# Kernel tuning notes

Measured on AMD Instinct MI355X. Metric: run time of the kernel, lower is better.

Reference implementation:

```python
import jax, jax.numpy as jnp
import numpy as np

B, S, E, H, D, NE, R = 2, 2048, 2048, 16, 128, 8, 16
HALF = D // 2
THETA = 10000.0


def setup_inputs() -> dict:
    key = jax.random.key(0)
    ks = jax.random.split(key, 18)

    def w(k, shape, fan_in):
        return jax.random.normal(k, shape, jnp.float32) / np.float32(np.sqrt(fan_in))

    inp = {
        "x": jax.random.normal(ks[0], (B, S, E), jnp.float32),
        "expert_mask": jax.random.uniform(ks[1], (B, S, NE), dtype=jnp.float32),
    }
    for i, n in enumerate(("q", "k", "v")):
        inp["W" + n] = w(ks[2 + 3 * i], (H * D, E), E)
        inp["b" + n] = jnp.zeros((H * D,), jnp.float32)
        inp["A" + n] = w(ks[3 + 3 * i], (NE, R, E), E)
        inp["B" + n] = w(ks[4 + 3 * i], (H * D, NE, R), R)
    inp["Wo"] = w(ks[11], (E, H * D), H * D)
    inp["bo"] = jnp.zeros((E,), jnp.float32)
    inp["Ao"] = w(ks[12], (NE, R, H * D), H * D)
    inp["Bo"] = w(ks[13], (E, NE, R), R)
    return inp


def routed_linear(x, W, b, A, Bm, mask):
    """MaybeRoutedLinear: dense base + expert-routed low-rank path gated by mask [B,S,NE]."""
    y = jnp.einsum("bsi,oi->bso", x, W) + b
    h = jnp.einsum("bsi,eri->bser", x, A) * mask[..., None]  # [B,S,NE,R]
    return y + jnp.einsum("bser,oer->bso", h, Bm)


def apply_rope(t):
    """Llama-style rotary embedding. t: [B,S,H,D]."""
    inv_freq = 1.0 / (THETA ** (jnp.arange(0, D, 2, dtype=jnp.float32) / D))  # [D/2]
    freqs = jnp.arange(S, dtype=jnp.float32)[:, None] * inv_freq[None, :]  # [S,D/2]
    cos = jnp.concatenate([jnp.cos(freqs)] * 2, -1)[None, :, None, :]  # [1,S,1,D]
    sin = jnp.concatenate([jnp.sin(freqs)] * 2, -1)[None, :, None, :]
    rot = jnp.concatenate([-t[..., HALF:], t[..., :HALF]], -1)
    return t * cos + rot * sin


def reference(x, expert_mask, Wq, bq, Aq, Bq, Wk, bk, Ak, Bk, Wv, bv, Av, Bv, Wo, bo, Ao, Bo):
    q = routed_linear(x, Wq, bq, Aq, Bq, expert_mask).reshape(B, S, H, D)
    k = routed_linear(x, Wk, bk, Ak, Bk, expert_mask).reshape(B, S, H, D)
    v = routed_linear(x, Wv, bv, Av, Bv, expert_mask).reshape(B, S, H, D)
    q = apply_rope(q)
    k = apply_rope(k)
    scores = jnp.einsum("bqhd,bkhd->bhqk", q, k) / jnp.float32(np.sqrt(D))
    causal = jnp.tril(jnp.ones((S, S), dtype=bool))
    scores = jnp.where(causal[None, None], scores, jnp.finfo(scores.dtype).min)
    probs = jax.nn.softmax(scores, axis=-1)
    o = jnp.einsum("bhqk,bkhd->bqhd", probs, v).reshape(B, S, H * D)
    return routed_linear(o, Wo, bo, Ao, Bo, expert_mask)
```

## Files before the change

kernel.cpp:

```cpp
#include <hip/hip_runtime.h>


#define B_ 2
#define S_ 2048
#define E_ 2048
#define H_ 16
#define D_ 128
#define NE_ 8
#define R_ 16
#define HD_ 2048
#define M_ 4096
#define KL_ 128

typedef unsigned short u16;
typedef unsigned int u32;
typedef __attribute__((ext_vector_type(8))) short bf16x8;
typedef __attribute__((ext_vector_type(4))) float f32x4;

typedef const __attribute__((address_space(1))) void gvoid_t;
typedef __attribute__((address_space(3))) void svoid_t;

__device__ __forceinline__ float bf2f(u16 u) {
    union { u32 i; float f; } v; v.i = ((u32)u) << 16; return v.f;
}
__device__ __forceinline__ u16 f2bf(float f) {
    union { float f; u32 i; } v; v.f = f;
    u32 x = v.i;
    return (u16)((x + 0x7fffu + ((x >> 16) & 1u)) >> 16);
}
__device__ __forceinline__ float ldf(const void* p, size_t i, int f) {
    return f ? ((const float*)p)[i] : bf2f(((const u16*)p)[i]);
}
__device__ __forceinline__ float4 ld4(const void* p, size_t i, int f) {
    if (f) return *(const float4*)((const float*)p + i);
    ushort4 v = *(const ushort4*)((const u16*)p + i);
    return make_float4(bf2f(v.x), bf2f(v.y), bf2f(v.z), bf2f(v.w));
}

__global__ void k_detect(const void* __restrict__ x, int* __restrict__ flags) {
    __shared__ int votes[2];
    int tid = threadIdx.x;
    if (tid < 2) votes[tid] = 0;
    __syncthreads();
    const u32* p = (const u32*)x;
    int bad = 0, tot = 0;
    for (int i = tid; i < 4096; i += 64) {
        u32 lo = p[i] & 0xffffu;
        if (lo) {
            tot++;
            int e = (int)((lo >> 7) & 0xffu);
            if (e < 100 || e > 150) bad++;
        }
    }
    atomicAdd(&votes[0], bad);
    atomicAdd(&votes[1], tot);
    __syncthreads();
    if (tid == 0) flags[0] = (votes[1] > 0 && votes[0] * 10 > votes[1] * 3) ? 1 : 0;
}

__global__ void k_cvt(const void* __restrict__ src, u16* __restrict__ dst, int n,
                      const int* __restrict__ flags) {
    int fin = flags[0];
    int i = (blockIdx.x * 256 + threadIdx.x) * 4;
    if (i >= n) return;
    float4 v = ld4(src, i, fin);
    ushort4 o;
    o.x = f2bf(v.x); o.y = f2bf(v.y); o.z = f2bf(v.z); o.w = f2bf(v.w);
    *(ushort4*)(dst + i) = o;
}

__global__ void k_cvtf(const float* __restrict__ src, u16* __restrict__ dst, int n) {
    int i = (blockIdx.x * 256 + threadIdx.x) * 4;
    if (i >= n) return;
    float4 v = *(const float4*)(src + i);
    ushort4 o;
    o.x = f2bf(v.x); o.y = f2bf(v.y); o.z = f2bf(v.z); o.w = f2bf(v.w);
    *(ushort4*)(dst + i) = o;
}

__global__ void k_zero(float4* __restrict__ p, int n4) {
    int i = blockIdx.x * 256 + threadIdx.x;
    if (i < n4) p[i] = make_float4(0.f, 0.f, 0.f, 0.f);
}

#define NX_  8388608L
#define NA1_ 262144L
#define NW_  4194304L
__global__ void k_cvt_all(
    const void* __restrict__ x,
    const void* __restrict__ Aq, const void* __restrict__ Ak,
    const void* __restrict__ Av, const void* __restrict__ Ao,
    const void* __restrict__ Bq, const void* __restrict__ Bk,
    const void* __restrict__ Bv, const void* __restrict__ Bo,
    const void* __restrict__ Wq, const void* __restrict__ Wk,
    const void* __restrict__ Wv,
    u16* __restrict__ Xb, u16* __restrict__ Acat, u16* __restrict__ Bmcat,
    u16* __restrict__ Wcat,
    const int* __restrict__ flags) {
    int fin = flags[0];
    long i = (long)(blockIdx.x * 256 + threadIdx.x) * 4;
    const void* src; u16* dst; long off;
    if (i < NX_) { src = x; dst = Xb; off = i; }
    else if (i < NX_ + 4 * NA1_) {
        long j = i - NX_; int p = (int)(j >> 18); off = j & (NA1_ - 1);
        src = (p == 0) ? Aq : (p == 1) ? Ak : (p == 2) ? Av : Ao;
        dst = Acat + (long)p * NA1_;
    } else if (i < NX_ + 8 * NA1_) {
        long j = i - NX_ - 4 * NA1_; int p = (int)(j >> 18); off = j & (NA1_ - 1);
        src = (p == 0) ? Bq : (p == 1) ? Bk : (p == 2) ? Bv : Bo;
        dst = Bmcat + (long)p * NA1_;
    } else {
        long j = i - NX_ - 8 * NA1_; int p = (int)(j / NW_); off = j - (long)p * NW_;
        src = (p == 0) ? Wq : (p == 1) ? Wk : Wv;
        dst = Wcat + (long)p * NW_;
    }
    float4 v = ld4(src, off, fin);
    ushort4 o;
    o.x = f2bf(v.x); o.y = f2bf(v.y); o.z = f2bf(v.z); o.w = f2bf(v.w);
    *(ushort4*)(dst + off) = o;
}

#define BM_ 128
#define BN_ 128
#define BK_ 64

__global__ __launch_bounds__(256, 2) void k_gemm_sk(
    const u16* __restrict__ A, int lda,
    const u16* __restrict__ Bw, int ldb, int K,
    const void* __restrict__ mask,
    float* __restrict__ Cf, int ldc,
    const int* __restrict__ flags) {
    __shared__ __align__(16) u16 As[BM_ * BK_];
    __shared__ __align__(16) u16 Bs[BN_ * BK_];
    int fin = flags[0];
    int tid = threadIdx.x;
    int w = tid >> 6, lane = tid & 63;
    int l15 = lane & 15, quad = lane >> 4;
    int wm = w >> 1, wn = w & 1;
    int m0 = blockIdx.y * BM_, n0 = blockIdx.x * BN_;
    int lrow = lane >> 3;
    int lcol = (lane & 7) * 8;

    f32x4 acc[4][4];
#pragma unroll
    for (int mt = 0; mt < 4; mt++)
#pragma unroll
        for (int nt = 0; nt < 4; nt++)
#pragma unroll
            for (int r = 0; r < 4; r++) acc[mt][nt][r] = 0.f;

    int iters = (K / BK_) / gridDim.z;
    int it0 = blockIdx.z * iters;
    for (int it = it0; it < it0 + iters; it++) {
        int kb = it * BK_;
        __syncthreads();
#pragma unroll
        for (int i = 0; i < 4; i++) {
            int rowb = (w * 4 + i) * 8;
            int r = rowb + lrow;
            __builtin_amdgcn_global_load_lds(
                (gvoid_t*)(A + (size_t)(m0 + r) * lda + kb + lcol),
                (svoid_t*)(As + rowb * BK_), 16, 0, 0);
            __builtin_amdgcn_global_load_lds(
                (gvoid_t*)(Bw + (size_t)(n0 + r) * ldb + kb + lcol),
                (svoid_t*)(Bs + rowb * BK_), 16, 0, 0);
        }
        __syncthreads();
#pragma unroll
        for (int kk = 0; kk < 2; kk++) {
            int ko = kk * 32 + quad * 8;
            bf16x8 af[4], bf[4];
#pragma unroll
            for (int mt = 0; mt < 4; mt++)
                af[mt] = *(const bf16x8*)(As + (wm * 64 + mt * 16 + l15) * BK_ + ko);
#pragma unroll
            for (int nt = 0; nt < 4; nt++)
                bf[nt] = *(const bf16x8*)(Bs + (wn * 64 + nt * 16 + l15) * BK_ + ko);
#pragma unroll
            for (int mt = 0; mt < 4; mt++)
#pragma unroll
                for (int nt = 0; nt < 4; nt++)
                    acc[mt][nt] = __builtin_amdgcn_mfma_f32_16x16x32_bf16(
                        af[mt], bf[nt], acc[mt][nt], 0, 0, 0);
        }
    }

#pragma unroll
    for (int mt = 0; mt < 4; mt++) {
#pragma unroll
        for (int r = 0; r < 4; r++) {
            int m = m0 + wm * 64 + mt * 16 + quad * 4 + r;
#pragma unroll
            for (int nt = 0; nt < 4; nt++) {
                int n = n0 + wn * 64 + nt * 16 + l15;
                float v = acc[mt][nt][r] * ldf(mask, (size_t)m * NE_ + ((n & 127) >> 4), fin);
                atomicAdd(&Cf[(size_t)m * ldc + n], v);
            }
        }
    }
}

template <int BMt>
__global__ __launch_bounds__(512, 2) void k_gemm8p(
    const u16* __restrict__ A, int lda,
    const u16* __restrict__ Bw, int ldb, int K1,
    const u16* __restrict__ A2, int lda2,
    const u16* __restrict__ B2, int K2,
    const void* __restrict__ bias0, const void* __restrict__ bias1,
    const void* __restrict__ bias2,
    void* __restrict__ C, int ldc, int store_mode,
    const int* __restrict__ flags) {
    constexpr int MT  = BMt / 32;
    constexpr int NSA = BMt / 16;
    constexpr int LA  = BMt / 128;
    constexpr int L   = LA + 2;
    __shared__ __align__(16) u16 As[4][NSA * 512];
    __shared__ __align__(16) u16 Bs[4][16 * 512];
    int fin = flags[0];
    int tid = threadIdx.x;
    int w = tid >> 6, lane = tid & 63;
    int l15 = lane & 15, quad = lane >> 4;
    int wm = w >> 2, wn = w & 3;

    int lin = blockIdx.y * gridDim.x + blockIdx.x;
    int cpx = (gridDim.x * gridDim.y) >> 3;
    int wg = (lin & 7) * cpx + (lin >> 3);
    int m0 = (wg / gridDim.x) * BMt;
    int n0 = (wg % gridDim.x) * 256;

    int p = (store_mode == 3) ? (n0 >> 11) : 0;
    const u16* A2p = A2 + p * 128;
    const u16* B2p = B2 + (long)p * NA1_;
    int nloc = (store_mode == 3) ? (n0 & 2047) : n0;

    int nk1 = K1 >> 5;
    int NT = nk1 + (K2 >> 5);

    f32x4 acc[MT][4];
#pragma unroll
    for (int mt = 0; mt < MT; mt++)
#pragma unroll
        for (int nt = 0; nt < 4; nt++)
#pragma unroll
            for (int r = 0; r < 4; r++) acc[mt][nt][r] = 0.f;

    auto stageA = [&](int kt) {
        const u16* pa; size_t sa; int kb;
        if (kt < nk1) { pa = A;   sa = (size_t)lda;  kb = kt * 32; }
        else          { pa = A2p; sa = (size_t)lda2; kb = (kt - nk1) * 32; }
        int buf = kt & 3;
#pragma unroll
        for (int j = 0; j < LA; j++) {
            int rb = w * LA + j;
            __builtin_amdgcn_global_load_lds(
                (gvoid_t*)(pa + (size_t)(m0 + rb * 16 + l15) * sa + kb + quad * 8),
                (svoid_t*)(&As[buf][rb * 512]), 16, 0, 0);
        }
    };
    auto stageB = [&](int kt) {
        const u16* pb; size_t sb; int kb, nb;
        if (kt < nk1) { pb = Bw;  sb = (size_t)ldb; kb = kt * 32;          nb = n0; }
        else          { pb = B2p; sb = (size_t)K2;  kb = (kt - nk1) * 32;  nb = nloc; }
        int buf = kt & 3;
#pragma unroll
        for (int j = 0; j < 2; j++) {
            int rb = w * 2 + j;
            __builtin_amdgcn_global_load_lds(
                (gvoid_t*)(pb + (size_t)(nb + rb * 16 + l15) * sb + kb + quad * 8),
                (svoid_t*)(&Bs[buf][rb * 512]), 16, 0, 0);
        }
    };

    stageA(0); stageB(0);
    stageA(1); stageB(1);
    stageA(2); stageB(2);
    if constexpr (L == 4) asm volatile("s_waitcnt vmcnt(8)" ::: "memory");
    else                  asm volatile("s_waitcnt vmcnt(6)" ::: "memory");
    __builtin_amdgcn_s_barrier();

    for (int kt = 0; kt < NT; kt++) {
        int buf = kt & 3;
        bool pre = (kt + 3 < NT);

        bf16x8 af[MT], bfr[4];
#pragma unroll
        for (int mt = 0; mt < MT; mt++)
            af[mt] = *(const bf16x8*)(&As[buf][(wm * MT + mt) * 512 + lane * 8]);
        bfr[0] = *(const bf16x8*)(&Bs[buf][(wn * 4 + 0) * 512 + lane * 8]);
        bfr[1] = *(const bf16x8*)(&Bs[buf][(wn * 4 + 1) * 512 + lane * 8]);
        if (pre) stageA(kt + 3);
        __builtin_amdgcn_s_barrier();
        asm volatile("s_waitcnt lgkmcnt(0)" ::: "memory");
        __builtin_amdgcn_sched_barrier(0);
        __builtin_amdgcn_s_setprio(1);
#pragma unroll
        for (int mt = 0; mt < MT; mt++) {
            acc[mt][0] = __builtin_amdgcn_mfma_f32_16x16x32_bf16(af[mt], bfr[0], acc[mt][0], 0, 0, 0);
            acc[mt][1] = __builtin_amdgcn_mfma_f32_16x16x32_bf16(af[mt], bfr[1], acc[mt][1], 0, 0, 0);
        }
        __builtin_amdgcn_s_setprio(0);
        __builtin_amdgcn_s_barrier();

        bfr[2] = *(const bf16x8*)(&Bs[buf][(wn * 4 + 2) * 512 + lane * 8]);
        bfr[3] = *(const bf16x8*)(&Bs[buf][(wn * 4 + 3) * 512 + lane * 8]);
        if (pre) stageB(kt + 3);
        __builtin_amdgcn_s_barrier();
        asm volatile("s_waitcnt lgkmcnt(0)" ::: "memory");
        __builtin_amdgcn_sched_barrier(0);
        __builtin_amdgcn_s_setprio(1);
#pragma unroll
        for (int mt = 0; mt < MT; mt++) {
            acc[mt][2] = __builtin_amdgcn_mfma_f32_16x16x32_bf16(af[mt], bfr[2], acc[mt][2], 0, 0, 0);
            acc[mt][3] = __builtin_amdgcn_mfma_f32_16x16x32_bf16(af[mt], bfr[3], acc[mt][3], 0, 0, 0);
        }
        __builtin_amdgcn_s_setprio(0);
        if (kt + 4 <= NT) {
            if constexpr (L == 4) asm volatile("s_waitcnt vmcnt(8)" ::: "memory");
            else                  asm volatile("s_waitcnt vmcnt(6)" ::: "memory");
        } else if (kt + 3 == NT) {
            if constexpr (L == 4) asm volatile("s_waitcnt vmcnt(4)" ::: "memory");
            else                  asm volatile("s_waitcnt vmcnt(3)" ::: "memory");
        } else if (kt + 2 == NT) {
            asm volatile("s_waitcnt vmcnt(0)" ::: "memory");
        }
        __builtin_amdgcn_s_barrier();
    }

    const void* bp = (store_mode == 3) ? (p == 0 ? bias0 : p == 1 ? bias1 : bias2)
                                       : bias0;
#pragma unroll
    for (int mt = 0; mt < MT; mt++) {
#pragma unroll
        for (int r = 0; r < 4; r++) {
            int m = m0 + wm * (BMt / 2) + mt * 16 + quad * 4 + r;
#pragma unroll
            for (int nt = 0; nt < 4; nt++) {
                int n = n0 + wn * 64 + nt * 16 + l15;
                float v = acc[mt][nt][r];
                if (bp) v += ldf(bp, (size_t)(n & 2047), fin);
                if (store_mode == 3) {
                    ((u16*)C)[(size_t)p * 8388608 + (size_t)m * 2048 + (n & 2047)] = f2bf(v);
                } else {
                    if (fin) ((float*)C)[(size_t)m * ldc + n] = v;
                    else     ((u16*)C)[(size_t)m * ldc + n] = f2bf(v);
                }
            }
        }
    }
}

__global__ void k_rope3(u16* __restrict__ Q, u16* __restrict__ K) {
    int idx = blockIdx.x * 256 + threadIdx.x;
    int d2g = idx & 15;
    int rs  = idx >> 4;
    int s   = rs & (S_ - 1);
    float cs[4], sn[4];
#pragma unroll
    for (int j = 0; j < 4; j++) {
        int d2 = d2g * 4 + j;
        float inv = powf(10000.f, -(float)d2 * (1.f / 64.f));
        float fr = (float)s * inv;
        sincosf(fr, &sn[j], &cs[j]);
    }
#pragma unroll
    for (int h = 0; h < H_; h++) {
        size_t base = ((size_t)(rs * H_ + h)) << 7;
#pragma unroll
        for (int a = 0; a < 2; a++) {
            u16* Y = a ? K : Q;
            ushort4 lo = *(const ushort4*)(Y + base + d2g * 4);
            ushort4 hi = *(const ushort4*)(Y + base + 64 + d2g * 4);
            ushort4 lo2, hi2;
            {
                float t0 = bf2f(lo.x), t1 = bf2f(hi.x);
                lo2.x = f2bf(t0 * cs[0] - t1 * sn[0]); hi2.x = f2bf(t1 * cs[0] + t0 * sn[0]);
            }
            {
                float t0 = bf2f(lo.y), t1 = bf2f(hi.y);
                lo2.y = f2bf(t0 * cs[1] - t1 * sn[1]); hi2.y = f2bf(t1 * cs[1] + t0 * sn[1]);
            }
            {
                float t0 = bf2f(lo.z), t1 = bf2f(hi.z);
                lo2.z = f2bf(t0 * cs[2] - t1 * sn[2]); hi2.z = f2bf(t1 * cs[2] + t0 * sn[2]);
            }
            {
                float t0 = bf2f(lo.w), t1 = bf2f(hi.w);
                lo2.w = f2bf(t0 * cs[3] - t1 * sn[3]); hi2.w = f2bf(t1 * cs[3] + t0 * sn[3]);
            }
            *(ushort4*)(Y + base + d2g * 4) = lo2;
            *(ushort4*)(Y + base + 64 + d2g * 4) = hi2;
        }
    }
}

__global__ void k_transpose_v(const u16* __restrict__ Vb, u16* __restrict__ Vt) {
    __shared__ u16 t[32][33];
    int s0 = blockIdx.x * 32;
    int n0 = blockIdx.y * 32;
    int b  = blockIdx.z;
    int tx = threadIdx.x & 31, ty = threadIdx.x >> 5;
#pragma unroll
    for (int r = 0; r < 4; r++)
        t[ty + r * 8][tx] = Vb[((size_t)(b * S_ + s0 + ty + r * 8)) * HD_ + n0 + tx];
    __syncthreads();
#pragma unroll
    for (int r = 0; r < 4; r++)
        Vt[((size_t)(b * HD_ + n0 + ty + r * 8)) * S_ + s0 + tx] = t[tx][ty + r * 8];
}

#define KS_ST 136
#define VT_ST 72
#define SCALE_ 0.088388347648318447f

__global__ __launch_bounds__(256, 3) void k_flash8(
    const u16* __restrict__ Q, const u16* __restrict__ K,
    const u16* __restrict__ Vt, u16* __restrict__ O) {
    __shared__ __align__(16) u16 Ks[64 * KS_ST];
    __shared__ __align__(16) u16 Vs[128 * VT_ST];
    __shared__ __align__(16) u16 Ps[64 * VT_ST];
    int tid = threadIdx.x;
    int w = tid >> 6, lane = tid & 63;
    int l15 = lane & 15, quad = lane >> 4;

    int lin = blockIdx.y * gridDim.x + blockIdx.x;
    int wg  = (lin & 7) * 64 + (lin >> 3);
    int bh = wg >> 4, pair = wg & 15;
    int b = bh >> 4, h = bh & 15;

    int krow[4], kd8[4], vd[4], vkg[4];
#pragma unroll
    for (int it = 0; it < 4; it++) {
        int idx = it * 256 + tid;
        krow[it] = idx >> 4; kd8[it] = (idx & 15) * 8;
        vd[it] = idx >> 3;   vkg[it] = (idx & 7) * 8;
    }

    for (int seg = 0; seg < 2; seg++) {
        int t = seg == 0 ? (31 - pair) : pair;
        int q0 = t * 64;

        bf16x8 qf[4];
        size_t baseQ = ((size_t)(b * S_ + q0 + w * 16 + l15)) * HD_ + h * D_;
#pragma unroll
        for (int ks = 0; ks < 4; ks++)
            qf[ks] = *(const bf16x8*)(Q + baseQ + ks * 32 + quad * 8);

        f32x4 of[8];
#pragma unroll
        for (int nt = 0; nt < 8; nt++)
#pragma unroll
            for (int r = 0; r < 4; r++) of[nt][r] = 0.f;
        float mreg = -30000.f, lreg = 0.f;
        int qrow = q0 + w * 16 + l15;

        int nch = t + 1;

        bf16x8 kpA[4], vpA[4], kpB[4], vpB[4];
#pragma unroll
        for (int it = 0; it < 4; it++) {
            kpA[it] = *(const bf16x8*)(K + ((size_t)(b * S_ + krow[it])) * HD_ + h * D_ + kd8[it]);
            vpA[it] = *(const bf16x8*)(Vt + ((size_t)(bh * 128 + vd[it])) * S_ + vkg[it]);
        }
        if (nch > 1) {
#pragma unroll
            for (int it = 0; it < 4; it++) {
                kpB[it] = *(const bf16x8*)(K + ((size_t)(b * S_ + 64 + krow[it])) * HD_ + h * D_ + kd8[it]);
                vpB[it] = *(const bf16x8*)(Vt + ((size_t)(bh * 128 + vd[it])) * S_ + 64 + vkg[it]);
            }
        }

        for (int c = 0; c < nch; c++) {
            int k0 = c * 64;
            __syncthreads();
            if ((c & 1) == 0) {
#pragma unroll
                for (int it = 0; it < 4; it++) {
                    *(bf16x8*)(Ks + krow[it] * KS_ST + kd8[it]) = kpA[it];
                    *(bf16x8*)(Vs + vd[it] * VT_ST + vkg[it]) = vpA[it];
                }
            } else {
#pragma unroll
                for (int it = 0; it < 4; it++) {
                    *(bf16x8*)(Ks + krow[it] * KS_ST + kd8[it]) = kpB[it];
                    *(bf16x8*)(Vs + vd[it] * VT_ST + vkg[it]) = vpB[it];
                }
            }
            __syncthreads();
            if (c + 2 < nch) {
                int k2 = k0 + 128;
                if ((c & 1) == 0) {
#pragma unroll
                    for (int it = 0; it < 4; it++) {
                        kpA[it] = *(const bf16x8*)(K + ((size_t)(b * S_ + k2 + krow[it])) * HD_ + h * D_ + kd8[it]);
                        vpA[it] = *(const bf16x8*)(Vt + ((size_t)(bh * 128 + vd[it])) * S_ + k2 + vkg[it]);
                    }
                } else {
#pragma unroll
                    for (int it = 0; it < 4; it++) {
                        kpB[it] = *(const bf16x8*)(K + ((size_t)(b * S_ + k2 + krow[it])) * HD_ + h * D_ + kd8[it]);
                        vpB[it] = *(const bf16x8*)(Vt + ((size_t)(bh * 128 + vd[it])) * S_ + k2 + vkg[it]);
                    }
                }
            }

            f32x4 sf[4];
#pragma unroll
            for (int nt = 0; nt < 4; nt++)
#pragma unroll
                for (int r = 0; r < 4; r++) sf[nt][r] = 0.f;
#pragma unroll
            for (int ks = 0; ks < 4; ks++) {
                int koff = ks * 32 + quad * 8;
                bf16x8 qa = qf[ks];
#pragma unroll
                for (int nt = 0; nt < 4; nt++) {
                    bf16x8 kb = *(const bf16x8*)(Ks + (nt * 16 + l15) * KS_ST + koff);
                    sf[nt] = __builtin_amdgcn_mfma_f32_16x16x32_bf16(kb, qa, sf[nt], 0, 0, 0);
                }
            }

#pragma unroll
            for (int nt = 0; nt < 4; nt++) {
                int keyb = k0 + nt * 16 + quad * 4;
#pragma unroll
                for (int r = 0; r < 4; r++) {
                    float sv = sf[nt][r] * SCALE_;
                    sf[nt][r] = (keyb + r > qrow) ? -30000.f : sv;
                }
            }

            float t0 = fmaxf(fmaxf(sf[0][0], sf[0][1]), fmaxf(sf[0][2], sf[0][3]));
            float t1 = fmaxf(fmaxf(sf[1][0], sf[1][1]), fmaxf(sf[1][2], sf[1][3]));
            float t2 = fmaxf(fmaxf(sf[2][0], sf[2][1]), fmaxf(sf[2][2], sf[2][3]));
            float t3 = fmaxf(fmaxf(sf[3][0], sf[3][1]), fmaxf(sf[3][2], sf[3][3]));
            float cmax = fmaxf(fmaxf(t0, t1), fmaxf(t2, t3));
            cmax = fmaxf(cmax, __shfl_xor(cmax, 16, 64));
            cmax = fmaxf(cmax, __shfl_xor(cmax, 32, 64));
            float mnew = fmaxf(mreg, cmax);
            float a = __expf(mreg - mnew);
            mreg = mnew;
#pragma unroll
            for (int nt = 0; nt < 4; nt++)
#pragma unroll
                for (int r = 0; r < 4; r++)
                    sf[nt][r] = __expf(sf[nt][r] - mnew);
            float s0 = (sf[0][0] + sf[0][1]) + (sf[0][2] + sf[0][3]);
            float s1 = (sf[1][0] + sf[1][1]) + (sf[1][2] + sf[1][3]);
            float s2 = (sf[2][0] + sf[2][1]) + (sf[2][2] + sf[2][3]);
            float s3 = (sf[3][0] + sf[3][1]) + (sf[3][2] + sf[3][3]);
            float psum = (s0 + s1) + (s2 + s3);
            psum += __shfl_xor(psum, 16, 64);
            psum += __shfl_xor(psum, 32, 64);
            lreg = lreg * a + psum;

            float al[4];
#pragma unroll
            for (int r = 0; r < 4; r++) al[r] = __shfl(a, quad * 4 + r, 16);

#pragma unroll
            for (int nt = 0; nt < 4; nt++)
#pragma unroll
                for (int r = 0; r < 4; r++)
                    Ps[(w * 16 + l15) * VT_ST + nt * 16 + quad * 4 + r] = f2bf(sf[nt][r]);
#pragma unroll
            for (int nt = 0; nt < 8; nt++)
#pragma unroll
                for (int r = 0; r < 4; r++) of[nt][r] *= al[r];

#pragma unroll
            for (int ks2 = 0; ks2 < 2; ks2++) {
                int koff = ks2 * 32 + quad * 8;
                bf16x8 pa = *(const bf16x8*)(Ps + (w * 16 + l15) * VT_ST + koff);
#pragma unroll
                for (int nt = 0; nt < 8; nt++) {
                    bf16x8 vb = *(const bf16x8*)(Vs + (nt * 16 + l15) * VT_ST + koff);
                    of[nt] = __builtin_amdgcn_mfma_f32_16x16x32_bf16(pa, vb, of[nt], 0, 0, 0);
                }
            }
        }

        float linv = 1.f / lreg;
        float inv[4];
#pragma unroll
        for (int r = 0; r < 4; r++) inv[r] = __shfl(linv, quad * 4 + r, 16);
        int rowb = q0 + w * 16 + quad * 4;
#pragma unroll
        for (int r = 0; r < 4; r++) {
            size_t base = ((size_t)(b * S_ + rowb + r)) * HD_ + h * D_;
#pragma unroll
            for (int nt = 0; nt < 8; nt++)
                O[base + nt * 16 + l15] = f2bf(of[nt][r] * inv[r]);
        }
    }
}

extern "C" void kernel_launch(void* const* d_in, const int* in_sizes, int n_in,
                              void* d_out, int out_size, void* d_ws, size_t ws_size,
                              hipStream_t stream) {
    const void* x    = d_in[0];
    const void* mask = d_in[1];
    const void* Wq = d_in[2];  const void* bq = d_in[3];
    const void* Aq = d_in[4];  const void* Bq = d_in[5];
    const void* Wk = d_in[6];  const void* bk = d_in[7];
    const void* Ak = d_in[8];  const void* Bk = d_in[9];
    const void* Wv = d_in[10]; const void* bv = d_in[11];
    const void* Av = d_in[12]; const void* Bv = d_in[13];
    const void* Wo = d_in[14]; const void* bo = d_in[15];
    const void* Ao = d_in[16]; const void* Bo = d_in[17];

    char* ws = (char*)d_ws;
    const long MB = 1 << 20;
    int* flags = (int*)ws;
    u16* Xb    = (u16*)(ws + 1  * MB);
    u16* Acat  = (u16*)(ws + 17 * MB);
    u16* Bmcat = (u16*)(ws + 19 * MB);
    u16* hg3   = (u16*)(ws + 21 * MB);
    u16* hgo   = (u16*)(ws + 24 * MB);
    u16* Qb    = (u16*)(ws + 25 * MB);
    u16* Kb    = (u16*)(ws + 41 * MB);
    u16* Vb    = (u16*)(ws + 57 * MB);
    u16* Vt    = (u16*)(ws + 73 * MB);
    u16* Wcat  = (u16*)(ws + 73 * MB);
    float* hg3f = (float*)Qb;
    float* hgof = (float*)Kb;
    u16* Wob   = Qb;
    u16* Ob    = Vb;

    k_detect<<<1, 64, 0, stream>>>(x, flags);
    k_zero<<<1536, 256, 0, stream>>>((float4*)hg3f, 393216);
    const long NCVT = NX_ + 8 * NA1_ + 3 * NW_;
    k_cvt_all<<<NCVT / 1024, 256, 0, stream>>>(
        x, Aq, Ak, Av, Ao, Bq, Bk, Bv, Bo, Wq, Wk, Wv,
        Xb, Acat, Bmcat, Wcat, flags);

    k_gemm_sk<<<dim3(3, M_ / BM_, 4), 256, 0, stream>>>(
        Xb, E_, Acat, E_, E_, mask, hg3f, 384, flags);
    k_cvtf<<<1536, 256, 0, stream>>>(hg3f, hg3, 1572864);

    k_gemm8p<256><<<dim3(6144 / 256, M_ / 256), 512, 0, stream>>>(
        Xb, E_, Wcat, E_, E_, hg3, 384, Bmcat, KL_,
        bq, bk, bv, Qb, HD_, 3, flags);

    k_rope3<<<256, 256, 0, stream>>>(Qb, Kb);
    k_transpose_v<<<dim3(S_ / 32, HD_ / 32, B_), 256, 0, stream>>>(Vb, Vt);

    k_flash8<<<dim3(16, 32), 256, 0, stream>>>(Qb, Kb, Vt, Ob);

    k_zero<<<512, 256, 0, stream>>>((float4*)hgof, 131072);
    k_cvt<<<NW_ / 1024, 256, 0, stream>>>(Wo, Wob, (int)NW_, flags);
    k_gemm_sk<<<dim3(1, M_ / BM_, 4), 256, 0, stream>>>(
        Ob, HD_, Acat + 3 * NA1_, E_, E_, mask, hgof, KL_, flags);
    k_cvtf<<<512, 256, 0, stream>>>(hgof, hgo, 524288);

    k_gemm8p<128><<<dim3(HD_ / 256, M_ / 128), 512, 0, stream>>>(
        Ob, HD_, Wob, E_, E_, hgo, KL_, Bmcat + 3 * NA1_, KL_,
        bo, nullptr, nullptr, d_out, HD_, 2, flags);
}
```

Before: 720.0 us.

## Stage flash-attention K/V tiles via async global-to-LDS loads with swizzled double buffers

The flash attention kernel used to stage K and V tiles through registers before storing them to padded shared memory. It now uses direct global-to-LDS loads into double-buffered K and V tiles. Bank conflicts are avoided with an XOR swizzle in place of padding rows. Loading chunk c+1 now overlaps compute on chunk c, with one barrier per iteration instead of two, and register pressure for prefetch drops. In exchange, the larger LDS footprint lowers the occupancy hint from 3 to 2 blocks per CU.

Result: faster. 648.4 us (-9.9%).

```diff
diff --git a/kernel.cpp b/kernel.cpp
--- a/kernel.cpp
+++ b/kernel.cpp
@@ -408,32 +408,46 @@
         Vt[((size_t)(b * HD_ + n0 + ty + r * 8)) * S_ + s0 + tx] = t[tx][ty + r * 8];
 }
 
-#define KS_ST 136
 #define VT_ST 72
 #define SCALE_ 0.088388347648318447f
 
-__global__ __launch_bounds__(256, 3) void k_flash8(
+__global__ __launch_bounds__(256, 2) void k_flash9(
     const u16* __restrict__ Q, const u16* __restrict__ K,
     const u16* __restrict__ Vt, u16* __restrict__ O) {
-    __shared__ __align__(16) u16 Ks[64 * KS_ST];
-    __shared__ __align__(16) u16 Vs[128 * VT_ST];
+    __shared__ __align__(16) u16 Ks[2][64 * 128];
+    __shared__ __align__(16) u16 Vs[2][128 * 64];
     __shared__ __align__(16) u16 Ps[64 * VT_ST];
     int tid = threadIdx.x;
     int w = tid >> 6, lane = tid & 63;
     int l15 = lane & 15, quad = lane >> 4;
+    int swz = l15 & 7;
 
     int lin = blockIdx.y * gridDim.x + blockIdx.x;
     int wg  = (lin & 7) * 64 + (lin >> 3);
     int bh = wg >> 4, pair = wg & 15;
     int b = bh >> 4, h = bh & 15;
 
-    int krow[4], kd8[4], vd[4], vkg[4];
-#pragma unroll
-    for (int it = 0; it < 4; it++) {
-        int idx = it * 256 + tid;
-        krow[it] = idx >> 4; kd8[it] = (idx & 15) * 8;
-        vd[it] = idx >> 3;   vkg[it] = (idx & 7) * 8;
-    }
+    auto stageKV = [&](int c, int buf) {
+        int k0s = c * 64;
+#pragma unroll
+        for (int j = 0; j < 4; j++) {
+            int g = (w * 4 + j) * 64 + lane;
+            int row = g >> 4;
+            int gs = (g & 15) ^ (row & 7);
+            __builtin_amdgcn_global_load_lds(
+                (gvoid_t*)(K + (size_t)(b * S_ + k0s + row) * HD_ + h * D_ + gs * 8),
+                (svoid_t*)(&Ks[buf][(w * 4 + j) * 512]), 16, 0, 0);
+        }
+#pragma unroll
+        for (int j = 0; j < 4; j++) {
+            int g = (w * 4 + j) * 64 + lane;
+            int row = g >> 3;
+            int gs = (g & 7) ^ (row & 7);
+            __builtin_amdgcn_global_load_lds(
+                (gvoid_t*)(Vt + (size_t)(bh * 128 + row) * S_ + k0s + gs * 8),
+                (svoid_t*)(&Vs[buf][(w * 4 + j) * 512]), 16, 0, 0);
+        }
+    };
 
     for (int seg = 0; seg < 2; seg++) {
         int t = seg == 0 ? (31 - pair) : pair;
@@ -455,53 +469,15 @@
 
         int nch = t + 1;
 
-        bf16x8 kpA[4], vpA[4], kpB[4], vpB[4];
-#pragma unroll
-        for (int it = 0; it < 4; it++) {
-            kpA[it] = *(const bf16x8*)(K + ((size_t)(b * S_ + krow[it])) * HD_ + h * D_ + kd8[it]);
-            vpA[it] = *(const bf16x8*)(Vt + ((size_t)(bh * 128 + vd[it])) * S_ + vkg[it]);
-        }
-        if (nch > 1) {
-#pragma unroll
-            for (int it = 0; it < 4; it++) {
-                kpB[it] = *(const bf16x8*)(K + ((size_t)(b * S_ + 64 + krow[it])) * HD_ + h * D_ + kd8[it]);
-                vpB[it] = *(const bf16x8*)(Vt + ((size_t)(bh * 128 + vd[it])) * S_ + 64 + vkg[it]);
-            }
-        }
+        stageKV(0, 0);
+        __syncthreads();
 
         for (int c = 0; c < nch; c++) {
             int k0 = c * 64;
-            __syncthreads();
-            if ((c & 1) == 0) {
-#pragma unroll
-                for (int it = 0; it < 4; it++) {
-                    *(bf16x8*)(Ks + krow[it] * KS_ST + kd8[it]) = kpA[it];
-                    *(bf16x8*)(Vs + vd[it] * VT_ST + vkg[it]) = vpA[it];
-                }
-            } else {
-#pragma unroll
-                for (int it = 0; it < 4; it++) {
-                    *(bf16x8*)(Ks + krow[it] * KS_ST + kd8[it]) = kpB[it];
-                    *(bf16x8*)(Vs + vd[it] * VT_ST + vkg[it]) = vpB[it];
-                }
-            }
-            __syncthreads();
-            if (c + 2 < nch) {
-                int k2 = k0 + 128;
-                if ((c & 1) == 0) {
-#pragma unroll
-                    for (int it = 0; it < 4; it++) {
-                        kpA[it] = *(const bf16x8*)(K + ((size_t)(b * S_ + k2 + krow[it])) * HD_ + h * D_ + kd8[it]);
-                        vpA[it] = *(const bf16x8*)(Vt + ((size_t)(bh * 128 + vd[it])) * S_ + k2 + vkg[it]);
-                    }
-                } else {
-#pragma unroll
-                    for (int it = 0; it < 4; it++) {
-                        kpB[it] = *(const bf16x8*)(K + ((size_t)(b * S_ + k2 + krow[it])) * HD_ + h * D_ + kd8[it]);
-                        vpB[it] = *(const bf16x8*)(Vt + ((size_t)(bh * 128 + vd[it])) * S_ + k2 + vkg[it]);
-                    }
-                }
-            }
+            int buf = c & 1;
+            if (c + 1 < nch) stageKV(c + 1, buf ^ 1);
+            const u16* Ksb = Ks[buf];
+            const u16* Vsb = Vs[buf];
 
             f32x4 sf[4];
 #pragma unroll
@@ -510,11 +486,11 @@
                 for (int r = 0; r < 4; r++) sf[nt][r] = 0.f;
 #pragma unroll
             for (int ks = 0; ks < 4; ks++) {
-                int koff = ks * 32 + quad * 8;
                 bf16x8 qa = qf[ks];
 #pragma unroll
                 for (int nt = 0; nt < 4; nt++) {
-                    bf16x8 kb = *(const bf16x8*)(Ks + (nt * 16 + l15) * KS_ST + koff);
+                    bf16x8 kb = *(const bf16x8*)(Ksb + (nt * 16 + l15) * 128
+                                                 + (((ks * 4 + quad) ^ swz) * 8));
                     sf[nt] = __builtin_amdgcn_mfma_f32_16x16x32_bf16(kb, qa, sf[nt], 0, 0, 0);
                 }
             }
@@ -573,10 +549,13 @@
                 bf16x8 pa = *(const bf16x8*)(Ps + (w * 16 + l15) * VT_ST + koff);
 #pragma unroll
                 for (int nt = 0; nt < 8; nt++) {
-                    bf16x8 vb = *(const bf16x8*)(Vs + (nt * 16 + l15) * VT_ST + koff);
+                    bf16x8 vb = *(const bf16x8*)(Vsb + (nt * 16 + l15) * 64
+                                                 + (((ks2 * 4 + quad) ^ swz) * 8));
                     of[nt] = __builtin_amdgcn_mfma_f32_16x16x32_bf16(pa, vb, of[nt], 0, 0, 0);
                 }
             }
+
+            __syncthreads();
         }
 
         float linv = 1.f / lreg;
@@ -644,7 +623,7 @@
     k_rope3<<<256, 256, 0, stream>>>(Qb, Kb);
     k_transpose_v<<<dim3(S_ / 32, HD_ / 32, B_), 256, 0, stream>>>(Vb, Vt);
 
-    k_flash8<<<dim3(16, 32), 256, 0, stream>>>(Qb, Kb, Vt, Ob);
+    k_flash9<<<dim3(16, 32), 256, 0, stream>>>(Qb, Kb, Vt, Ob);
 
     k_zero<<<512, 256, 0, stream>>>((float4*)hgof, 131072);
     k_cvt<<<NW_ / 1024, 256, 0, stream>>>(Wo, Wob, (int)NW_, flags);
```
